# Kernel tuning notes

Hardware: AMD Instinct MI355X
Metric: run time of the kernel (lower is better)

The kernel has to match this reference:

```python
import jax, jax.numpy as jnp
import numpy as np

B, T, HID = 2, 2048, 2048
H, KVH, D = 16, 4, 128
N_REP = H // KVH


def _rotate_half(x):
    x1, x2 = jnp.split(x, 2, axis=-1)
    return jnp.concatenate([-x2, x1], axis=-1)


def setup_inputs() -> dict:
    key = jax.random.key(0)
    ks = jax.random.split(key, 8)
    hidden_states = jax.random.normal(ks[0], (B, T, HID), dtype=jnp.float32)
    # RoPE tables: standard theta=10000 frequencies, emb = cat(freqs, freqs)
    inv_freq = 1.0 / (10000.0 ** (np.arange(0, D, 2, dtype=np.float32) / D))
    pos = np.arange(T, dtype=np.float32)
    freqs = np.outer(pos, inv_freq)                      # [T, D/2]
    emb = np.concatenate([freqs, freqs], axis=-1)        # [T, D]
    cos = jnp.broadcast_to(jnp.cos(emb)[None], (B, T, D)).astype(jnp.float32)
    sin = jnp.broadcast_to(jnp.sin(emb)[None], (B, T, D)).astype(jnp.float32)
    # causal additive mask [1,1,T,T]
    neg = jnp.finfo(jnp.float32).min
    causal = jnp.where(jnp.tril(jnp.ones((T, T), dtype=bool)), 0.0, neg)
    attention_mask = causal[None, None].astype(jnp.float32)
    s = 0.02
    Wq = jax.random.normal(ks[1], (H * D, HID), dtype=jnp.float32) * s
    Wk = jax.random.normal(ks[2], (KVH * D, HID), dtype=jnp.float32) * s
    Wv = jax.random.normal(ks[3], (KVH * D, HID), dtype=jnp.float32) * s
    Wo = jax.random.normal(ks[4], (HID, H * D), dtype=jnp.float32) * s
    bq = jnp.zeros((H * D,), dtype=jnp.float32)
    bk = jnp.zeros((KVH * D,), dtype=jnp.float32)
    bv = jnp.zeros((KVH * D,), dtype=jnp.float32)
    return {"hidden_states": hidden_states, "cos": cos, "sin": sin,
            "attention_mask": attention_mask,
            "Wq": Wq, "bq": bq, "Wk": Wk, "bk": bk, "Wv": Wv, "bv": bv, "Wo": Wo}


def reference(hidden_states, cos, sin, attention_mask, Wq, bq, Wk, bk, Wv, bv, Wo):
    bsz, q_len, _ = hidden_states.shape
    q = (jnp.einsum('bth,oh->bto', hidden_states, Wq) + bq).reshape(bsz, q_len, H, D).transpose(0, 2, 1, 3)
    k = (jnp.einsum('bth,oh->bto', hidden_states, Wk) + bk).reshape(bsz, q_len, KVH, D).transpose(0, 2, 1, 3)
    v = (jnp.einsum('bth,oh->bto', hidden_states, Wv) + bv).reshape(bsz, q_len, KVH, D).transpose(0, 2, 1, 3)
    c = cos[:, None, :, :]  # [B,1,T,D]
    s = sin[:, None, :, :]
    q = q * c + _rotate_half(q) * s
    k = k * c + _rotate_half(k) * s
    # repeat KV heads to match Q heads (GQA)
    k = jnp.repeat(k, N_REP, axis=1)  # [B,H,T,D]
    v = jnp.repeat(v, N_REP, axis=1)
    scores = jnp.einsum('bhqd,bhkd->bhqk', q, k) / jnp.sqrt(jnp.float32(D))
    scores = scores + attention_mask
    attn = jax.nn.softmax(scores.astype(jnp.float32), axis=-1).astype(q.dtype)
    out = jnp.einsum('bhqk,bhkd->bhqd', attn, v)          # [B,H,T,D]
    out = out.transpose(0, 2, 1, 3).reshape(bsz, q_len, H * D)
    return jnp.einsum('bto,ho->bth', out, Wo)
```

## Files before the change

kernel.cpp:

```cpp
#include <hip/hip_runtime.h>
#include <hip/hip_bf16.h>
#include <stdint.h>

#define B_ 2
#define T_ 2048
#define HID_ 2048
#define H_ 16
#define KVH_ 4
#define D_ 128

typedef __attribute__((ext_vector_type(8))) short short8;
typedef __attribute__((ext_vector_type(4))) float f32x4;

__device__ __forceinline__ uint16_t f2bf(float x) {
  union { float f; uint32_t u; } c; c.f = x;
  uint32_t r = c.u + 0x7fffu + ((c.u >> 16) & 1u);
  return (uint16_t)(r >> 16);
}
__device__ __forceinline__ float bf2f(uint16_t b) {
  union { uint32_t u; float f; } c; c.u = ((uint32_t)b) << 16;
  return c.f;
}
__device__ __forceinline__ uint16_t hwbf(float x) {
  __hip_bfloat16 h = __float2bfloat16(x);
  return *reinterpret_cast<uint16_t*>(&h);
}

#define XM(r) (((r) & 7) ^ (((r) >> 1) & 4))

__global__ __launch_bounds__(256) void cvt_f32_bf16(const float* __restrict__ in,
                                                    uint16_t* __restrict__ out, int n) {
  int i = (blockIdx.x * 256 + threadIdx.x) * 4;
  if (i >= n) return;
  const float4 v = *reinterpret_cast<const float4*>(in + i);
  union { uint16_t s[4]; uint2 u; } pk;
  pk.s[0] = f2bf(v.x); pk.s[1] = f2bf(v.y); pk.s[2] = f2bf(v.z); pk.s[3] = f2bf(v.w);
  *reinterpret_cast<uint2*>(out + i) = pk.u;
}

__global__ __launch_bounds__(256) void concat_bias(const float* __restrict__ bq,
                                                   const float* __restrict__ bk,
                                                   const float* __restrict__ bv,
                                                   float* __restrict__ out) {
  int i = blockIdx.x * 256 + threadIdx.x;
  if (i < 2048) out[i] = bq[i];
  else if (i < 2560) out[i] = bk[i - 2048];
  else if (i < 3072) out[i] = bv[i - 2560];
}

#define BM 128
#define BN 128
#define BK 64

template<bool OUT_F32, bool HAS_BIAS>
__global__ __launch_bounds__(256, 2) void gemm_bt(const uint16_t* __restrict__ A,
                                                  const uint16_t* __restrict__ Bt,
                                                  void* __restrict__ Cv,
                                                  const float* __restrict__ bias,
                                                  int M, int N, int K) {
  __shared__ __align__(16) uint16_t Al[2][BM * BK];
  __shared__ __align__(16) uint16_t Bl[2][BN * BK];
  const int tid = threadIdx.x;
  const int w = tid >> 6;
  const int lane = tid & 63;
  const int wr = w >> 1, wc = w & 1;
  const int lm = lane & 15, lg = lane >> 4;

  const int GX = gridDim.x;
  const int nwg = GX * gridDim.y;
  int bid = blockIdx.y * GX + blockIdx.x;
  bid = (bid & 7) * (nwg >> 3) + (bid >> 3);
  const int bm = (bid / GX) * BM;
  const int bn = (bid % GX) * BN;

  f32x4 acc[4][4];
  const f32x4 z4 = {0.f, 0.f, 0.f, 0.f};
#pragma unroll
  for (int i = 0; i < 4; ++i)
#pragma unroll
    for (int j = 0; j < 4; ++j) acc[i][j] = z4;

  const int nt = K >> 6;

  auto stage = [&](int b, int t) {
    const int k0 = t * BK;
#pragma unroll
    for (int it = 0; it < 4; ++it) {
      const int chunk = it * 256 + tid;
      const int r = chunk >> 3, c8 = chunk & 7;
      const int csw = (c8 ^ XM(r)) * 8;
      const uint16_t* gA = A + (size_t)(bm + r) * K + k0 + csw;
      const uint16_t* gB = Bt + (size_t)(bn + r) * K + k0 + csw;
      __builtin_amdgcn_global_load_lds((const __attribute__((address_space(1))) unsigned int*)gA,
                                       (__attribute__((address_space(3))) unsigned int*)(&Al[b][0] + chunk * 8),
                                       16, 0, 0);
      __builtin_amdgcn_global_load_lds((const __attribute__((address_space(1))) unsigned int*)gB,
                                       (__attribute__((address_space(3))) unsigned int*)(&Bl[b][0] + chunk * 8),
                                       16, 0, 0);
    }
  };

  stage(0, 0);
  __syncthreads();

  int cur = 0;
  for (int t = 0; t < nt; ++t) {
    if (t + 1 < nt) stage(cur ^ 1, t + 1);
#pragma unroll
    for (int kk = 0; kk < 2; ++kk) {
      short8 af[4], bfr[4];
#pragma unroll
      for (int mi = 0; mi < 4; ++mi) {
        const int r = wr * 64 + mi * 16 + lm;
        af[mi] = *reinterpret_cast<const short8*>(&Al[cur][r * BK + (((kk * 4 + lg) ^ XM(r)) * 8)]);
      }
#pragma unroll
      for (int ni = 0; ni < 4; ++ni) {
        const int r = wc * 64 + ni * 16 + lm;
        bfr[ni] = *reinterpret_cast<const short8*>(&Bl[cur][r * BK + (((kk * 4 + lg) ^ XM(r)) * 8)]);
      }
#pragma unroll
      for (int mi = 0; mi < 4; ++mi)
#pragma unroll
        for (int ni = 0; ni < 4; ++ni)
          acc[mi][ni] = __builtin_amdgcn_mfma_f32_16x16x32_bf16(af[mi], bfr[ni], acc[mi][ni], 0, 0, 0);
    }
    __syncthreads();
    cur ^= 1;
  }

#pragma unroll
  for (int mi = 0; mi < 4; ++mi) {
#pragma unroll
    for (int ni = 0; ni < 4; ++ni) {
      const int col = bn + wc * 64 + ni * 16 + lm;
      float bb = 0.f;
      if (HAS_BIAS) bb = bias[col];
#pragma unroll
      for (int r = 0; r < 4; ++r) {
        const int row = bm + wr * 64 + mi * 16 + lg * 4 + r;
        const float v = acc[mi][ni][r] + bb;
        if (OUT_F32) reinterpret_cast<float*>(Cv)[(size_t)row * N + col] = v;
        else reinterpret_cast<uint16_t*>(Cv)[(size_t)row * N + col] = f2bf(v);
      }
    }
  }
}

#define SC_Q 0.1275523865396698f

__global__ __launch_bounds__(320) void rope_scatter(const uint16_t* __restrict__ raw,
                                                    const float* __restrict__ cosp,
                                                    const float* __restrict__ sinp,
                                                    uint16_t* __restrict__ Qo,
                                                    uint16_t* __restrict__ Ko) {
  const int c8 = threadIdx.x;
  const int m = blockIdx.x;
  const int b = m >> 11, tt = m & 2047;
  const int c = c8 * 8;
  const int d = c & 127;
  const size_t rowoff = (size_t)m * 3072;
  union { short8 v; uint16_t s[8]; } x8, p8, o8;
  x8.v = *reinterpret_cast<const short8*>(raw + rowoff + c);
  p8.v = *reinterpret_cast<const short8*>(raw + rowoff + (c ^ 64));
  const float* cb = cosp + ((size_t)b * T_ + tt) * D_ + d;
  const float* sb = sinp + ((size_t)b * T_ + tt) * D_ + d;
  const bool isq = (c < 2048);
  const float scale = isq ? SC_Q : 1.0f;
  const float sgn = (d < 64) ? -1.f : 1.f;
#pragma unroll
  for (int j = 0; j < 8; ++j) {
    const float x = bf2f(x8.s[j]);
    const float px = bf2f(p8.s[j]);
    o8.s[j] = f2bf((x * cb[j] + sgn * px * sb[j]) * scale);
  }
  if (isq) {
    const int hh = c >> 7;
    *reinterpret_cast<short8*>(Qo + (((size_t)(b * H_ + hh)) * T_ + tt) * D_ + d) = o8.v;
  } else {
    const int hh = (c - 2048) >> 7;
    *reinterpret_cast<short8*>(Ko + (((size_t)(b * KVH_ + hh)) * T_ + tt) * D_ + d) = o8.v;
  }
}

__global__ __launch_bounds__(256) void transpose_v(const uint16_t* __restrict__ raw,
                                                   uint16_t* __restrict__ VtG) {
  const int hb = blockIdx.y;
  const int b = hb >> 2, kvh = hb & 3;
  const int d = threadIdx.x & 127;
  const int tw = threadIdx.x >> 7;
  const int t0 = blockIdx.x * 16 + tw * 8;
  const uint16_t* src = raw + ((size_t)(b * T_ + t0)) * 3072 + 2560 + kvh * 128 + d;
  union { uint16_t s[8]; short8 v; } pk;
#pragma unroll
  for (int j = 0; j < 8; ++j) pk.s[j] = src[(size_t)j * 3072];
  *reinterpret_cast<short8*>(VtG + ((size_t)hb * D_ + d) * T_ + t0) = pk.v;
}

#define KVBLK 64

__global__ __launch_bounds__(256, 2) void attn_fwd(const uint16_t* __restrict__ Qb,
                                                   const uint16_t* __restrict__ Kb,
                                                   const uint16_t* __restrict__ VtG,
                                                   uint16_t* __restrict__ Ab) {
  __shared__ __align__(16) uint16_t Kl[2][KVBLK * D_];
  __shared__ __align__(16) uint16_t Vtl[2][D_ * KVBLK];
  __shared__ __align__(16) uint16_t Pl[4 * 16 * 64];
  const int tid = threadIdx.x;
  const int w = tid >> 6, lane = tid & 63;
  const int lm = lane & 15, lg = lane >> 4;
  const int bh = blockIdx.y;
  const int b = bh >> 4, h = bh & 15;
  const int kvh = h >> 2;
  const int qtA = (blockIdx.x + bh) & 15;
  const int qtB = 31 - qtA;
  const int nA = qtA + 1;
  const int ntot = 33;

  const uint16_t* Kbase = Kb + ((size_t)(b * KVH_ + kvh)) * T_ * D_;
  const uint16_t* Vtbase = VtG + ((size_t)(b * KVH_ + kvh)) * D_ * T_;
  uint16_t* Pw = Pl + w * 16 * 64;
  const f32x4 z4 = {0.f, 0.f, 0.f, 0.f};

  short8 vone;
#pragma unroll
  for (int j = 0; j < 8; ++j) vone[j] = (short)0x3F80;

  f32x4 o[8];
  f32x4 osum;
  float mrow[4];
  short8 qf[4];

  auto loadQ = [&](int qt) {
    const uint16_t* Qw = Qb + (((size_t)(b * H_ + h)) * T_ + qt * 64 + w * 16) * D_;
#pragma unroll
    for (int kk = 0; kk < 4; ++kk)
      qf[kk] = *reinterpret_cast<const short8*>(Qw + (size_t)lm * D_ + kk * 32 + lg * 8);
  };
  auto resetAcc = [&]() {
#pragma unroll
    for (int f = 0; f < 8; ++f) o[f] = z4;
    osum = z4;
#pragma unroll
    for (int r = 0; r < 4; ++r) mrow[r] = -1e30f;
  };
  auto flush = [&](int qt) {
    const int wr0 = qt * 64 + w * 16;
    float rcp[4];
#pragma unroll
    for (int r = 0; r < 4; ++r) rcp[r] = 1.0f / osum[r];
#pragma unroll
    for (int f = 0; f < 8; ++f) {
      const int col = h * D_ + f * 16 + lm;
#pragma unroll
      for (int r = 0; r < 4; ++r) {
        const int trow = wr0 + lg * 4 + r;
        Ab[((size_t)(b * T_ + trow)) * (H_ * D_) + col] = f2bf(o[f][r] * rcp[r]);
      }
    }
  };
  auto stage = [&](int buf, int kv0) {
#pragma unroll
    for (int it = 0; it < 4; ++it) {
      const int chunk = it * 256 + tid;
      {
        const int r = chunk >> 4, c16 = chunk & 15;
        const uint16_t* g = Kbase + (size_t)(kv0 + r) * D_ + ((c16 ^ XM(r)) * 8);
        __builtin_amdgcn_global_load_lds((const __attribute__((address_space(1))) unsigned int*)g,
                                         (__attribute__((address_space(3))) unsigned int*)(&Kl[buf][0] + (it * 256 + w * 64) * 8),
                                         16, 0, 0);
      }
      {
        const int dd = chunk >> 3, c8 = chunk & 7;
        const uint16_t* g = Vtbase + (size_t)dd * T_ + kv0 + ((c8 ^ XM(dd)) * 8);
        __builtin_amdgcn_global_load_lds((const __attribute__((address_space(1))) unsigned int*)g,
                                         (__attribute__((address_space(3))) unsigned int*)(&Vtl[buf][0] + (it * 256 + w * 64) * 8),
                                         16, 0, 0);
      }
    }
  };

  loadQ(qtA);
  resetAcc();
  stage(0, 0);
  __syncthreads();

  int cur = 0;
  for (int g = 0; g < ntot; ++g) {
    const bool inA = g < nA;
    const int t = inA ? g : g - nA;
    const int qt = inA ? qtA : qtB;
    const int kv0 = t * KVBLK;
    const int wrow0 = qt * 64 + w * 16;

    if (g + 1 < ntot) {
      const int gn = g + 1;
      const int kvn = (gn < nA ? gn : gn - nA) * KVBLK;
      stage(cur ^ 1, kvn);
    }

    f32x4 s[4];
#pragma unroll
    for (int nf = 0; nf < 4; ++nf) s[nf] = z4;
#pragma unroll
    for (int nf = 0; nf < 4; ++nf)
#pragma unroll
      for (int kk = 0; kk < 4; ++kk) {
        const int row = nf * 16 + lm;
        const short8 kf = *reinterpret_cast<const short8*>(&Kl[cur][row * D_ + (((kk * 4 + lg) ^ XM(row)) * 8)]);
        s[nf] = __builtin_amdgcn_mfma_f32_16x16x32_bf16(qf[kk], kf, s[nf], 0, 0, 0);
      }

    if (kv0 + KVBLK - 1 > wrow0) {
#pragma unroll
      for (int nf = 0; nf < 4; ++nf) {
        const int colg = kv0 + nf * 16 + lm;
#pragma unroll
        for (int r = 0; r < 4; ++r) {
          const int rowg = wrow0 + lg * 4 + r;
          if (colg > rowg) s[nf][r] = -1e30f;
        }
      }
    }

    float tmax[4];
#pragma unroll
    for (int r = 0; r < 4; ++r)
      tmax[r] = fmaxf(fmaxf(s[0][r], s[1][r]), fmaxf(s[2][r], s[3][r]));
    bool grow = false;
#pragma unroll
    for (int r = 0; r < 4; ++r) grow = grow || (tmax[r] > mrow[r] + 8.f);
    if (__any((int)grow)) {
#pragma unroll
      for (int r = 0; r < 4; ++r) {
        float v = tmax[r];
        v = fmaxf(v, __shfl_xor(v, 1));
        v = fmaxf(v, __shfl_xor(v, 2));
        v = fmaxf(v, __shfl_xor(v, 4));
        v = fmaxf(v, __shfl_xor(v, 8));
        const float nm = fmaxf(mrow[r], v);
        const float al = exp2f(mrow[r] - nm);
        mrow[r] = nm;
        osum[r] *= al;
#pragma unroll
        for (int f = 0; f < 8; ++f) o[f][r] *= al;
      }
    }
#pragma unroll
    for (int nf = 0; nf < 4; ++nf)
#pragma unroll
      for (int r = 0; r < 4; ++r) {
        const float p = exp2f(s[nf][r] - mrow[r]);
        const int prow = lg * 4 + r;
        const int pchunk = (nf * 2 + (lm >> 3)) ^ XM(prow);
        Pw[prow * 64 + pchunk * 8 + (lm & 7)] = hwbf(p);
      }
    asm volatile("s_waitcnt lgkmcnt(0)" ::: "memory");
    short8 pf[2];
#pragma unroll
    for (int ks = 0; ks < 2; ++ks)
      pf[ks] = *reinterpret_cast<const short8*>(Pw + lm * 64 + (((ks * 4 + lg) ^ XM(lm)) * 8));
#pragma unroll
    for (int ks = 0; ks < 2; ++ks)
      osum = __builtin_amdgcn_mfma_f32_16x16x32_bf16(pf[ks], vone, osum, 0, 0, 0);
#pragma unroll
    for (int f = 0; f < 8; ++f)
#pragma unroll
      for (int ks = 0; ks < 2; ++ks) {
        const int dd = f * 16 + lm;
        const short8 vf = *reinterpret_cast<const short8*>(&Vtl[cur][dd * KVBLK + (((ks * 4 + lg) ^ XM(dd)) * 8)]);
        o[f] = __builtin_amdgcn_mfma_f32_16x16x32_bf16(pf[ks], vf, o[f], 0, 0, 0);
      }

    __syncthreads();
    cur ^= 1;

    if (g == nA - 1) {
      flush(qtA);
      loadQ(qtB);
      resetAcc();
    }
  }
  flush(qtB);
}

extern "C" void kernel_launch(void* const* d_in, const int* in_sizes, int n_in,
                              void* d_out, int out_size, void* d_ws, size_t ws_size,
                              hipStream_t stream) {
  const float* hidden = (const float*)d_in[0];
  const float* cosp   = (const float*)d_in[1];
  const float* sinp   = (const float*)d_in[2];
  const float* Wq = (const float*)d_in[4];
  const float* bq = (const float*)d_in[5];
  const float* Wk = (const float*)d_in[6];
  const float* bk = (const float*)d_in[7];
  const float* Wv = (const float*)d_in[8];
  const float* bv = (const float*)d_in[9];
  const float* Wo = (const float*)d_in[10];

  char* ws = (char*)d_ws;
  uint16_t* hidb   = (uint16_t*)(ws);
  uint16_t* wqkv   = (uint16_t*)(ws + 16777216);
  uint16_t* wob    = (uint16_t*)(ws + 29360128);
  float*    biasq  = (float*)   (ws + 37748736);
  uint16_t* qkvraw = (uint16_t*)(ws + 37761024);
  uint16_t* Qb     = (uint16_t*)(ws + 62926848);
  uint16_t* Kb     = (uint16_t*)(ws + 79704064);
  uint16_t* VtG    = (uint16_t*)(ws + 83898368);
  uint16_t* Ab     = (uint16_t*)(ws + 88092672);

  cvt_f32_bf16<<<8192, 256, 0, stream>>>(hidden, hidb, 8388608);
  cvt_f32_bf16<<<4096, 256, 0, stream>>>(Wq, wqkv, 4194304);
  cvt_f32_bf16<<<1024, 256, 0, stream>>>(Wk, wqkv + 4194304, 1048576);
  cvt_f32_bf16<<<1024, 256, 0, stream>>>(Wv, wqkv + 5242880, 1048576);
  cvt_f32_bf16<<<4096, 256, 0, stream>>>(Wo, wob, 4194304);
  concat_bias<<<12, 256, 0, stream>>>(bq, bk, bv, biasq);

  gemm_bt<false, true><<<dim3(24, 32), 256, 0, stream>>>(hidb, wqkv, qkvraw, biasq, 4096, 3072, 2048);
  rope_scatter<<<4096, 320, 0, stream>>>(qkvraw, cosp, sinp, Qb, Kb);
  transpose_v<<<dim3(128, 8), 256, 0, stream>>>(qkvraw, VtG);
  attn_fwd<<<dim3(16, 32), 256, 0, stream>>>(Qb, Kb, VtG, Ab);
  gemm_bt<true, false><<<dim3(16, 32), 256, 0, stream>>>(Ab, wob, d_out, nullptr, 4096, 2048, 2048);
}
```

Baseline: 228.0 us.

## Fuse RoPE and V transpose into QKV GEMM epilogue; merge conversion kernels

The QKV projection GEMM now writes its output directly as roped, scaled Q and K in head-major layout and as transposed V. The column mapping of each warp is remapped so that a lane holds both halves of the rotate_half pair in registers. This removes the intermediate qkvraw buffer round trip and the separate rope_scatter and transpose_v kernels. Five fp32-to-bf16 conversion launches and the bias concatenation are merged into one kernel to cut launch overhead. The risk is that the epilogue now does scattered 2-byte stores and per-element cos/sin loads, which may coalesce worse.

```diff
diff --git a/kernel.cpp b/kernel.cpp
--- a/kernel.cpp
+++ b/kernel.cpp
@@ -27,39 +27,52 @@
 }
 
 #define XM(r) (((r) & 7) ^ (((r) >> 1) & 4))
-
-__global__ __launch_bounds__(256) void cvt_f32_bf16(const float* __restrict__ in,
-                                                    uint16_t* __restrict__ out, int n) {
-  int i = (blockIdx.x * 256 + threadIdx.x) * 4;
-  if (i >= n) return;
-  const float4 v = *reinterpret_cast<const float4*>(in + i);
+#define SC_Q 0.1275523865396698f
+
+__global__ __launch_bounds__(256) void cvt_all(const float* __restrict__ hidden,
+                                               const float* __restrict__ Wq,
+                                               const float* __restrict__ Wk,
+                                               const float* __restrict__ Wv,
+                                               const float* __restrict__ Wo,
+                                               const float* __restrict__ bq,
+                                               const float* __restrict__ bk,
+                                               const float* __restrict__ bv,
+                                               uint16_t* __restrict__ hidb,
+                                               uint16_t* __restrict__ wqkv,
+                                               uint16_t* __restrict__ wob,
+                                               float* __restrict__ biasq) {
+  const int gtid = blockIdx.x * 256 + threadIdx.x;
+  const int i = gtid * 4;
+  const float* src;
+  uint16_t* dst;
+  if (i < 8388608)       { src = hidden + i;            dst = hidb + i; }
+  else if (i < 12582912) { src = Wq + (i - 8388608);    dst = wqkv + (i - 8388608); }
+  else if (i < 13631488) { src = Wk + (i - 12582912);   dst = wqkv + 4194304 + (i - 12582912); }
+  else if (i < 14680064) { src = Wv + (i - 13631488);   dst = wqkv + 5242880 + (i - 13631488); }
+  else                   { src = Wo + (i - 14680064);   dst = wob + (i - 14680064); }
+  const float4 v = *reinterpret_cast<const float4*>(src);
   union { uint16_t s[4]; uint2 u; } pk;
   pk.s[0] = f2bf(v.x); pk.s[1] = f2bf(v.y); pk.s[2] = f2bf(v.z); pk.s[3] = f2bf(v.w);
-  *reinterpret_cast<uint2*>(out + i) = pk.u;
-}
-
-__global__ __launch_bounds__(256) void concat_bias(const float* __restrict__ bq,
-                                                   const float* __restrict__ bk,
-                                                   const float* __restrict__ bv,
-                                                   float* __restrict__ out) {
-  int i = blockIdx.x * 256 + threadIdx.x;
-  if (i < 2048) out[i] = bq[i];
-  else if (i < 2560) out[i] = bk[i - 2048];
-  else if (i < 3072) out[i] = bv[i - 2560];
+  *reinterpret_cast<uint2*>(dst) = pk.u;
+  if (gtid < 3072)
+    biasq[gtid] = (gtid < 2048) ? bq[gtid] : (gtid < 2560) ? bk[gtid - 2048] : bv[gtid - 2560];
 }
 
 #define BM 128
 #define BN 128
 #define BK 64
 
-template<bool OUT_F32, bool HAS_BIAS>
-__global__ __launch_bounds__(256, 2) void gemm_bt(const uint16_t* __restrict__ A,
-                                                  const uint16_t* __restrict__ Bt,
-                                                  void* __restrict__ Cv,
-                                                  const float* __restrict__ bias,
-                                                  int M, int N, int K) {
+__global__ __launch_bounds__(256, 2) void gemm_qkv(const uint16_t* __restrict__ A,
+                                                   const uint16_t* __restrict__ Bt,
+                                                   const float* __restrict__ bias,
+                                                   const float* __restrict__ cosp,
+                                                   const float* __restrict__ sinp,
+                                                   uint16_t* __restrict__ Qo,
+                                                   uint16_t* __restrict__ Ko,
+                                                   uint16_t* __restrict__ VtG) {
   __shared__ __align__(16) uint16_t Al[2][BM * BK];
   __shared__ __align__(16) uint16_t Bl[2][BN * BK];
+  const int K = 2048;
   const int tid = threadIdx.x;
   const int w = tid >> 6;
   const int lane = tid & 63;
@@ -72,6 +85,8 @@
   bid = (bid & 7) * (nwg >> 3) + (bid >> 3);
   const int bm = (bid / GX) * BM;
   const int bn = (bid % GX) * BN;
+
+  const int colb[4] = {wc * 32, wc * 32 + 16, wc * 32 + 64, wc * 32 + 80};
 
   f32x4 acc[4][4];
   const f32x4 z4 = {0.f, 0.f, 0.f, 0.f};
@@ -116,7 +131,7 @@
       }
 #pragma unroll
       for (int ni = 0; ni < 4; ++ni) {
-        const int r = wc * 64 + ni * 16 + lm;
+        const int r = colb[ni] + lm;
         bfr[ni] = *reinterpret_cast<const short8*>(&Bl[cur][r * BK + (((kk * 4 + lg) ^ XM(r)) * 8)]);
       }
 #pragma unroll
@@ -129,72 +144,140 @@
     cur ^= 1;
   }
 
+  float bb[4];
+#pragma unroll
+  for (int ni = 0; ni < 4; ++ni) bb[ni] = bias[bn + colb[ni] + lm];
+
+  if (bn < 2560) {
+    const bool isQ = (bn < 2048);
+    const int head = isQ ? (bn >> 7) : ((bn - 2048) >> 7);
+    const int nh = isQ ? H_ : KVH_;
+    uint16_t* dst = isQ ? Qo : Ko;
+    const float sc = isQ ? SC_Q : 1.0f;
+#pragma unroll
+    for (int mi = 0; mi < 4; ++mi) {
+#pragma unroll
+      for (int r = 0; r < 4; ++r) {
+        const int row = bm + wr * 64 + mi * 16 + lg * 4 + r;
+        const int b = row >> 11, tt = row & 2047;
+        const float* cr = cosp + ((size_t)b * T_ + tt) * D_;
+        const float* sr = sinp + ((size_t)b * T_ + tt) * D_;
+        uint16_t* drow = dst + (((size_t)(b * nh + head)) * T_ + tt) * D_;
+#pragma unroll
+        for (int ni = 0; ni < 4; ++ni) {
+          const int d = colb[ni] + lm;
+          const float xv = acc[mi][ni][r] + bb[ni];
+          const float pv = acc[mi][ni ^ 2][r] + bb[ni ^ 2];
+          const float sgn = (ni < 2) ? -1.f : 1.f;
+          drow[d] = f2bf((xv * cr[d] + sgn * pv * sr[d]) * sc);
+        }
+      }
+    }
+  } else {
+    const int kvh = (bn - 2560) >> 7;
+#pragma unroll
+    for (int mi = 0; mi < 4; ++mi) {
+      const int row0 = bm + wr * 64 + mi * 16 + lg * 4;
+      const int b = row0 >> 11, t0 = row0 & 2047;
+#pragma unroll
+      for (int ni = 0; ni < 4; ++ni) {
+        const int d = colb[ni] + lm;
+        union { uint16_t s[4]; uint2 u; } pk;
+#pragma unroll
+        for (int r = 0; r < 4; ++r) pk.s[r] = f2bf(acc[mi][ni][r] + bb[ni]);
+        *reinterpret_cast<uint2*>(VtG + ((size_t)(b * KVH_ + kvh) * D_ + d) * T_ + t0) = pk.u;
+      }
+    }
+  }
+}
+
+__global__ __launch_bounds__(256, 2) void gemm_bt(const uint16_t* __restrict__ A,
+                                                  const uint16_t* __restrict__ Bt,
+                                                  float* __restrict__ Cv,
+                                                  int M, int N, int K) {
+  __shared__ __align__(16) uint16_t Al[2][BM * BK];
+  __shared__ __align__(16) uint16_t Bl[2][BN * BK];
+  const int tid = threadIdx.x;
+  const int w = tid >> 6;
+  const int lane = tid & 63;
+  const int wr = w >> 1, wc = w & 1;
+  const int lm = lane & 15, lg = lane >> 4;
+
+  const int GX = gridDim.x;
+  const int nwg = GX * gridDim.y;
+  int bid = blockIdx.y * GX + blockIdx.x;
+  bid = (bid & 7) * (nwg >> 3) + (bid >> 3);
+  const int bm = (bid / GX) * BM;
+  const int bn = (bid % GX) * BN;
+
+  f32x4 acc[4][4];
+  const f32x4 z4 = {0.f, 0.f, 0.f, 0.f};
+#pragma unroll
+  for (int i = 0; i < 4; ++i)
+#pragma unroll
+    for (int j = 0; j < 4; ++j) acc[i][j] = z4;
+
+  const int nt = K >> 6;
+
+  auto stage = [&](int b, int t) {
+    const int k0 = t * BK;
+#pragma unroll
+    for (int it = 0; it < 4; ++it) {
+      const int chunk = it * 256 + tid;
+      const int r = chunk >> 3, c8 = chunk & 7;
+      const int csw = (c8 ^ XM(r)) * 8;
+      const uint16_t* gA = A + (size_t)(bm + r) * K + k0 + csw;
+      const uint16_t* gB = Bt + (size_t)(bn + r) * K + k0 + csw;
+      __builtin_amdgcn_global_load_lds((const __attribute__((address_space(1))) unsigned int*)gA,
+                                       (__attribute__((address_space(3))) unsigned int*)(&Al[b][0] + chunk * 8),
+                                       16, 0, 0);
+      __builtin_amdgcn_global_load_lds((const __attribute__((address_space(1))) unsigned int*)gB,
+                                       (__attribute__((address_space(3))) unsigned int*)(&Bl[b][0] + chunk * 8),
+                                       16, 0, 0);
+    }
+  };
+
+  stage(0, 0);
+  __syncthreads();
+
+  int cur = 0;
+  for (int t = 0; t < nt; ++t) {
+    if (t + 1 < nt) stage(cur ^ 1, t + 1);
+#pragma unroll
+    for (int kk = 0; kk < 2; ++kk) {
+      short8 af[4], bfr[4];
+#pragma unroll
+      for (int mi = 0; mi < 4; ++mi) {
+        const int r = wr * 64 + mi * 16 + lm;
+        af[mi] = *reinterpret_cast<const short8*>(&Al[cur][r * BK + (((kk * 4 + lg) ^ XM(r)) * 8)]);
+      }
+#pragma unroll
+      for (int ni = 0; ni < 4; ++ni) {
+        const int r = wc * 64 + ni * 16 + lm;
+        bfr[ni] = *reinterpret_cast<const short8*>(&Bl[cur][r * BK + (((kk * 4 + lg) ^ XM(r)) * 8)]);
+      }
+#pragma unroll
+      for (int mi = 0; mi < 4; ++mi)
+#pragma unroll
+        for (int ni = 0; ni < 4; ++ni)
+          acc[mi][ni] = __builtin_amdgcn_mfma_f32_16x16x32_bf16(af[mi], bfr[ni], acc[mi][ni], 0, 0, 0);
+    }
+    __syncthreads();
+    cur ^= 1;
+  }
+
 #pragma unroll
   for (int mi = 0; mi < 4; ++mi) {
 #pragma unroll
     for (int ni = 0; ni < 4; ++ni) {
       const int col = bn + wc * 64 + ni * 16 + lm;
-      float bb = 0.f;
-      if (HAS_BIAS) bb = bias[col];
 #pragma unroll
       for (int r = 0; r < 4; ++r) {
         const int row = bm + wr * 64 + mi * 16 + lg * 4 + r;
-        const float v = acc[mi][ni][r] + bb;
-        if (OUT_F32) reinterpret_cast<float*>(Cv)[(size_t)row * N + col] = v;
-        else reinterpret_cast<uint16_t*>(Cv)[(size_t)row * N + col] = f2bf(v);
+        Cv[(size_t)row * N + col] = acc[mi][ni][r];
       }
     }
   }
-}
-
-#define SC_Q 0.1275523865396698f
-
-__global__ __launch_bounds__(320) void rope_scatter(const uint16_t* __restrict__ raw,
-                                                    const float* __restrict__ cosp,
-                                                    const float* __restrict__ sinp,
-                                                    uint16_t* __restrict__ Qo,
-                                                    uint16_t* __restrict__ Ko) {
-  const int c8 = threadIdx.x;
-  const int m = blockIdx.x;
-  const int b = m >> 11, tt = m & 2047;
-  const int c = c8 * 8;
-  const int d = c & 127;
-  const size_t rowoff = (size_t)m * 3072;
-  union { short8 v; uint16_t s[8]; } x8, p8, o8;
-  x8.v = *reinterpret_cast<const short8*>(raw + rowoff + c);
-  p8.v = *reinterpret_cast<const short8*>(raw + rowoff + (c ^ 64));
-  const float* cb = cosp + ((size_t)b * T_ + tt) * D_ + d;
-  const float* sb = sinp + ((size_t)b * T_ + tt) * D_ + d;
-  const bool isq = (c < 2048);
-  const float scale = isq ? SC_Q : 1.0f;
-  const float sgn = (d < 64) ? -1.f : 1.f;
-#pragma unroll
-  for (int j = 0; j < 8; ++j) {
-    const float x = bf2f(x8.s[j]);
-    const float px = bf2f(p8.s[j]);
-    o8.s[j] = f2bf((x * cb[j] + sgn * px * sb[j]) * scale);
-  }
-  if (isq) {
-    const int hh = c >> 7;
-    *reinterpret_cast<short8*>(Qo + (((size_t)(b * H_ + hh)) * T_ + tt) * D_ + d) = o8.v;
-  } else {
-    const int hh = (c - 2048) >> 7;
-    *reinterpret_cast<short8*>(Ko + (((size_t)(b * KVH_ + hh)) * T_ + tt) * D_ + d) = o8.v;
-  }
-}
-
-__global__ __launch_bounds__(256) void transpose_v(const uint16_t* __restrict__ raw,
-                                                   uint16_t* __restrict__ VtG) {
-  const int hb = blockIdx.y;
-  const int b = hb >> 2, kvh = hb & 3;
-  const int d = threadIdx.x & 127;
-  const int tw = threadIdx.x >> 7;
-  const int t0 = blockIdx.x * 16 + tw * 8;
-  const uint16_t* src = raw + ((size_t)(b * T_ + t0)) * 3072 + 2560 + kvh * 128 + d;
-  union { uint16_t s[8]; short8 v; } pk;
-#pragma unroll
-  for (int j = 0; j < 8; ++j) pk.s[j] = src[(size_t)j * 3072];
-  *reinterpret_cast<short8*>(VtG + ((size_t)hb * D_ + d) * T_ + t0) = pk.v;
 }
 
 #define KVBLK 64
@@ -403,22 +486,14 @@
   uint16_t* wqkv   = (uint16_t*)(ws + 16777216);
   uint16_t* wob    = (uint16_t*)(ws + 29360128);
   float*    biasq  = (float*)   (ws + 37748736);
-  uint16_t* qkvraw = (uint16_t*)(ws + 37761024);
   uint16_t* Qb     = (uint16_t*)(ws + 62926848);
   uint16_t* Kb     = (uint16_t*)(ws + 79704064);
   uint16_t* VtG    = (uint16_t*)(ws + 83898368);
   uint16_t* Ab     = (uint16_t*)(ws + 88092672);
 
-  cvt_f32_bf16<<<8192, 256, 0, stream>>>(hidden, hidb, 8388608);
-  cvt_f32_bf16<<<4096, 256, 0, stream>>>(Wq, wqkv, 4194304);
-  cvt_f32_bf16<<<1024, 256, 0, stream>>>(Wk, wqkv + 4194304, 1048576);
-  cvt_f32_bf16<<<1024, 256, 0, stream>>>(Wv, wqkv + 5242880, 1048576);
-  cvt_f32_bf16<<<4096, 256, 0, stream>>>(Wo, wob, 4194304);
-  concat_bias<<<12, 256, 0, stream>>>(bq, bk, bv, biasq);
-
-  gemm_bt<false, true><<<dim3(24, 32), 256, 0, stream>>>(hidb, wqkv, qkvraw, biasq, 4096, 3072, 2048);
-  rope_scatter<<<4096, 320, 0, stream>>>(qkvraw, cosp, sinp, Qb, Kb);
-  transpose_v<<<dim3(128, 8), 256, 0, stream>>>(qkvraw, VtG);
+  cvt_all<<<18432, 256, 0, stream>>>(hidden, Wq, Wk, Wv, Wo, bq, bk, bv,
+                                     hidb, wqkv, wob, biasq);
+  gemm_qkv<<<dim3(24, 32), 256, 0, stream>>>(hidb, wqkv, biasq, cosp, sinp, Qb, Kb, VtG);
   attn_fwd<<<dim3(16, 32), 256, 0, stream>>>(Qb, Kb, VtG, Ab);
-  gemm_bt<true, false><<<dim3(16, 32), 256, 0, stream>>>(Ab, wob, d_out, nullptr, 4096, 2048, 2048);
-}
+  gemm_bt<<<dim3(16, 32), 256, 0, stream>>>(Ab, wob, (float*)d_out, 4096, 2048, 2048);
+}
```

Result: faster. 211.1 us (-7.4%).
